# Optimization experiments

Measured on AMD Instinct MI355X. Metric: run time of the kernel, lower is better.

The kernel has to match this reference:

```python
import jax, jax.numpy as jnp
import numpy as np

N = 100000      # n_nodes
E = 1000000     # n_edges (avg degree 10)
D = 64          # input feature dim
LAT = 7         # latent_dim
R = 2           # perturb_rank
H = 2 * LAT     # GCN hidden / dense1 width = 14
P = (LAT + 1) * R  # dense2 width = 16
SP_INV_1 = float(np.log(np.expm1(1.0)))  # softplus_inverse(1.0)


def setup_inputs() -> dict:
    key = jax.random.key(0)
    ks = jax.random.split(key, 10)
    X = jax.random.normal(ks[0], (N, D), dtype=jnp.float32)
    rows = jax.random.randint(ks[1], (E,), 0, N, dtype=jnp.int32)
    cols = jax.random.randint(ks[2], (E,), 0, N, dtype=jnp.int32)
    vals = jax.random.uniform(ks[3], (E,), dtype=jnp.float32)
    s = 0.1
    W1 = jax.random.normal(ks[4], (D, H), dtype=jnp.float32) * s
    W2 = jax.random.normal(ks[5], (H, H), dtype=jnp.float32) * s
    Wd1 = jax.random.normal(ks[6], (H, H), dtype=jnp.float32) * s
    bd1 = jnp.zeros((H,), jnp.float32)
    Wd2 = jax.random.normal(ks[7], (H, P), dtype=jnp.float32) * s
    bd2 = jnp.zeros((P,), jnp.float32)
    return dict(X=X, rows=rows, cols=cols, vals=vals, W1=W1, W2=W2,
                Wd1=Wd1, bd1=bd1, Wd2=Wd2, bd2=bd2)


def reference(X, rows, cols, vals, W1, W2, Wd1, bd1, Wd2, bd2):
    # Sparse adjacency SpMM: (A @ F)[i] = sum_e vals[e] * F[cols[e]] for rows[e]==i
    def spmm(F):
        gathered = vals[:, None] * F[cols]          # [E, d] irregular gather
        return jax.ops.segment_sum(gathered, rows, num_segments=N)

    # GraphConvolution: relu(A @ X @ W)  (keras-gcn order: aggregate then transform)
    h = jax.nn.relu(spmm(X) @ W1)                   # [N, 14]
    h = jax.nn.relu(spmm(h) @ W2)                   # [N, 14]

    param_dist = jnp.tanh(h @ Wd1 + bd1)            # [N, 14]
    param_perturb = jnp.tanh(h @ Wd2 + bd2)         # [N, 16]

    loc = param_dist[:, :LAT]                                      # [N, 7]
    scale_diag = jax.nn.softplus(param_dist[:, LAT:] + SP_INV_1)   # [N, 7]
    perturb_U = param_perturb[:, :LAT * R]                         # [N, 14] (-> [N,7,2])
    perturb_m = param_perturb[:, LAT * R:]                         # [N, 2]

    # MVN-diag-plus-low-rank parameters, concatenated: [N, 7+7+14+2]
    return jnp.concatenate([loc, scale_diag, perturb_U, perturb_m], axis=-1)
```

## Files before the change

### kernel.cpp

```cpp
#include <hip/hip_runtime.h>
#include <hip/hip_fp16.h>
#include <math.h>

constexpr int D     = 64;
constexpr int H     = 14;
constexpr int HP2   = 8;
constexpr int P     = 16;
constexpr int LATc  = 7;
constexpr int OUTW  = 30;
constexpr float SP_INV_1 = 0.5413248546129181f;

__device__ __forceinline__ void pk_atomic_add_f16(__half2* addr, __half2 val) {
    unsigned int bits = *reinterpret_cast<unsigned int*>(&val);
    asm volatile("global_atomic_pk_add_f16 %0, %1, off"
                 :: "v"(addr), "v"(bits) : "memory");
}

__global__ void dense_xw_kernel(const float* __restrict__ X,
                                const float* __restrict__ W1,
                                __half2* __restrict__ XW,
                                __half2* __restrict__ Y1,
                                __half2* __restrict__ Y2, int N) {
    __shared__ float w[D * H];
    for (int i = threadIdx.x; i < D * H; i += blockDim.x) w[i] = W1[i];
    __syncthreads();
    int t = blockIdx.x * blockDim.x + threadIdx.x;
    int n = t >> 1;
    int half = t & 1;
    if (n >= N) return;

    float acc[H];
#pragma unroll
    for (int j = 0; j < H; ++j) acc[j] = 0.f;
    const float4* xr = reinterpret_cast<const float4*>(X + (size_t)n * D) + half * 8;
#pragma unroll
    for (int d4 = 0; d4 < 8; ++d4) {
        float4 x = xr[d4];
        float xs[4] = {x.x, x.y, x.z, x.w};
#pragma unroll
        for (int k = 0; k < 4; ++k) {
            int d = half * 32 + d4 * 4 + k;
#pragma unroll
            for (int j = 0; j < H; ++j) acc[j] = fmaf(xs[k], w[d * H + j], acc[j]);
        }
    }
#pragma unroll
    for (int j = 0; j < H; ++j) acc[j] += __shfl_xor(acc[j], 1);

    __half2 ov[4];
    if (half == 0) {
        ov[0] = __floats2half2_rn(acc[0], acc[1]);
        ov[1] = __floats2half2_rn(acc[2], acc[3]);
        ov[2] = __floats2half2_rn(acc[4], acc[5]);
        ov[3] = __floats2half2_rn(acc[6], acc[7]);
    } else {
        ov[0] = __floats2half2_rn(acc[8], acc[9]);
        ov[1] = __floats2half2_rn(acc[10], acc[11]);
        ov[2] = __floats2half2_rn(acc[12], acc[13]);
        ov[3] = __floats2half2_rn(0.f, 0.f);
    }
    reinterpret_cast<float4*>(XW + (size_t)n * HP2)[half] = *reinterpret_cast<float4*>(ov);

    float4 z = make_float4(0.f, 0.f, 0.f, 0.f);
    reinterpret_cast<float4*>(Y1 + (size_t)n * HP2)[half] = z;
    reinterpret_cast<float4*>(Y2 + (size_t)n * HP2)[half] = z;
}

__global__ void spmm_pk_kernel(const __half2* __restrict__ F,
                               const int* __restrict__ rows,
                               const int* __restrict__ cols,
                               const float* __restrict__ vals,
                               __half2* __restrict__ Y, int E) {
    int idx = blockIdx.x * blockDim.x + threadIdx.x;
    int e = idx >> 3;
    int f = idx & 7;
    if (e >= E || f >= 7) return;
    int r = rows[e];
    int c = cols[e];
    float v = vals[e];
    float2 xf = __half22float2(F[c * HP2 + f]);
    __half2 p = __floats2half2_rn(v * xf.x, v * xf.y);
    pk_atomic_add_f16(&Y[r * HP2 + f], p);
}

__global__ void dense_hw_kernel(const __half2* __restrict__ Y1,
                                const float* __restrict__ W2,
                                __half2* __restrict__ HW, int N) {
    __shared__ float w[H * H];
    for (int i = threadIdx.x; i < H * H; i += blockDim.x) w[i] = W2[i];
    __syncthreads();
    int n = blockIdx.x * blockDim.x + threadIdx.x;
    if (n >= N) return;
    const float4* yr4 = reinterpret_cast<const float4*>(Y1 + (size_t)n * HP2);
    float4 ya = yr4[0], yb = yr4[1];
    __half2 yh[HP2];
    *reinterpret_cast<float4*>(&yh[0]) = ya;
    *reinterpret_cast<float4*>(&yh[4]) = yb;
    float h[H];
#pragma unroll
    for (int k = 0; k < 7; ++k) {
        float2 t = __half22float2(yh[k]);
        h[2 * k]     = fmaxf(t.x, 0.f);
        h[2 * k + 1] = fmaxf(t.y, 0.f);
    }
    float o[H];
#pragma unroll
    for (int j = 0; j < H; ++j) {
        float a = 0.f;
#pragma unroll
        for (int i = 0; i < H; ++i) a = fmaf(h[i], w[i * H + j], a);
        o[j] = a;
    }
    __half2 ov[HP2];
#pragma unroll
    for (int j = 0; j < 7; ++j) ov[j] = __floats2half2_rn(o[2 * j], o[2 * j + 1]);
    ov[7] = __floats2half2_rn(0.f, 0.f);
    float4* dst = reinterpret_cast<float4*>(HW + (size_t)n * HP2);
    dst[0] = *reinterpret_cast<float4*>(&ov[0]);
    dst[1] = *reinterpret_cast<float4*>(&ov[4]);
}

__global__ __launch_bounds__(256) void final_kernel(
        const __half2* __restrict__ Y2,
        const float* __restrict__ Wd1,
        const float* __restrict__ bd1,
        const float* __restrict__ Wd2,
        const float* __restrict__ bd2,
        float* __restrict__ out, int N) {
    __shared__ float wd1[H * H], wd2[H * P], b1[H], b2[P];
    __shared__ float so[256 * OUTW];
    for (int i = threadIdx.x; i < H * H; i += 256) wd1[i] = Wd1[i];
    for (int i = threadIdx.x; i < H * P; i += 256) wd2[i] = Wd2[i];
    if (threadIdx.x < H) b1[threadIdx.x] = bd1[threadIdx.x];
    if (threadIdx.x < P) b2[threadIdx.x] = bd2[threadIdx.x];
    __syncthreads();

    int base = blockIdx.x * 256;
    int n = base + threadIdx.x;
    if (n < N) {
        const float4* yr4 = reinterpret_cast<const float4*>(Y2 + (size_t)n * HP2);
        float4 ya = yr4[0], yb = yr4[1];
        __half2 yh[HP2];
        *reinterpret_cast<float4*>(&yh[0]) = ya;
        *reinterpret_cast<float4*>(&yh[4]) = yb;
        float h[H];
#pragma unroll
        for (int k = 0; k < 7; ++k) {
            float2 t = __half22float2(yh[k]);
            h[2 * k]     = fmaxf(t.x, 0.f);
            h[2 * k + 1] = fmaxf(t.y, 0.f);
        }
        float* so_row = &so[threadIdx.x * OUTW];
        float pd7[LATc];
#pragma unroll
        for (int j = 0; j < H; ++j) {
            float a = b1[j];
#pragma unroll
            for (int i = 0; i < H; ++i) a = fmaf(h[i], wd1[i * H + j], a);
            float t = tanhf(a);
            if (j < LATc) so_row[j] = t;
            else pd7[j - LATc] = t;
        }
#pragma unroll
        for (int k = 0; k < LATc; ++k) {
            float x = pd7[k] + SP_INV_1;
            so_row[LATc + k] = log1pf(expf(x));
        }
#pragma unroll
        for (int j = 0; j < P; ++j) {
            float a = b2[j];
#pragma unroll
            for (int i = 0; i < H; ++i) a = fmaf(h[i], wd2[i * P + j], a);
            so_row[14 + j] = tanhf(a);
        }
    }
    __syncthreads();

    int rowsHere = N - base;
    if (rowsHere > 256) rowsHere = 256;
    if (rowsHere < 0) rowsHere = 0;
    int cnt = rowsHere * OUTW;
    float* obase = out + (size_t)base * OUTW;
    for (int i = threadIdx.x; i < cnt; i += 256) obase[i] = so[i];
}

extern "C" void kernel_launch(void* const* d_in, const int* in_sizes, int n_in,
                              void* d_out, int out_size, void* d_ws, size_t ws_size,
                              hipStream_t stream) {
    const float* X    = (const float*)d_in[0];
    const int*   rows = (const int*)d_in[1];
    const int*   cols = (const int*)d_in[2];
    const float* vals = (const float*)d_in[3];
    const float* W1   = (const float*)d_in[4];
    const float* W2   = (const float*)d_in[5];
    const float* Wd1  = (const float*)d_in[6];
    const float* bd1  = (const float*)d_in[7];
    const float* Wd2  = (const float*)d_in[8];
    const float* bd2  = (const float*)d_in[9];
    float* out = (float*)d_out;

    const int N = in_sizes[0] / D;
    const int E = in_sizes[1];

    __half2* XW = (__half2*)d_ws;
    __half2* HW = XW + (size_t)N * HP2;
    __half2* Y1 = HW + (size_t)N * HP2;
    __half2* Y2 = Y1 + (size_t)N * HP2;

    int blkN  = (N + 255) / 256;
    int blkN2 = (2 * N + 255) / 256;
    long long spmmThreads = (long long)E * 8;
    unsigned blkS = (unsigned)((spmmThreads + 255) / 256);

    dense_xw_kernel<<<blkN2, 256, 0, stream>>>(X, W1, XW, Y1, Y2, N);
    spmm_pk_kernel<<<blkS, 256, 0, stream>>>(XW, rows, cols, vals, Y1, E);
    dense_hw_kernel<<<blkN, 256, 0, stream>>>(Y1, W2, HW, N);
    spmm_pk_kernel<<<blkS, 256, 0, stream>>>(HW, rows, cols, vals, Y2, E);
    final_kernel<<<blkN, 256, 0, stream>>>(Y2, Wd1, bd1, Wd2, bd2, out, N);
}
```

Baseline: 219.0 us.

## Fuse both SpMM passes and dense W2 into persistent kernel with grid barrier

Replaces the two SpMM launches and the dense H×W2 kernel with one persistent kernel sized to occupancy. The kernel runs the first SpMM, waits on a global atomic barrier, then does the second SpMM with the W2 transform computed per edge on the gathered Y1 row instead of a separate pass. This removes two launches and the HW intermediate buffer. In exchange each edge recomputes a 14-wide dot product, reading all 7 half2 of the neighbor row per feature slot. The grid-wide spin barrier assumes every block is co-resident.

```diff
diff --git a/kernel.cpp b/kernel.cpp
--- a/kernel.cpp
+++ b/kernel.cpp
@@ -9,18 +9,24 @@
 constexpr int LATc  = 7;
 constexpr int OUTW  = 30;
 constexpr float SP_INV_1 = 0.5413248546129181f;
+constexpr int BLK   = 256;
 
 __device__ __forceinline__ void pk_atomic_add_f16(__half2* addr, __half2 val) {
     unsigned int bits = *reinterpret_cast<unsigned int*>(&val);
     asm volatile("global_atomic_pk_add_f16 %0, %1, off"
                  :: "v"(addr), "v"(bits) : "memory");
 }
+__device__ __forceinline__ unsigned int ld_agent(const unsigned int* p) {
+    return __hip_atomic_load(p, __ATOMIC_RELAXED, __HIP_MEMORY_SCOPE_AGENT);
+}
 
 __global__ void dense_xw_kernel(const float* __restrict__ X,
                                 const float* __restrict__ W1,
                                 __half2* __restrict__ XW,
                                 __half2* __restrict__ Y1,
-                                __half2* __restrict__ Y2, int N) {
+                                __half2* __restrict__ Y2,
+                                int* __restrict__ bar, int N) {
+    if (blockIdx.x == 0 && threadIdx.x == 0) *bar = 0;
     __shared__ float w[D * H];
     for (int i = threadIdx.x; i < D * H; i += blockDim.x) w[i] = W1[i];
     __syncthreads();
@@ -60,64 +66,82 @@
         ov[3] = __floats2half2_rn(0.f, 0.f);
     }
     reinterpret_cast<float4*>(XW + (size_t)n * HP2)[half] = *reinterpret_cast<float4*>(ov);
-
     float4 z = make_float4(0.f, 0.f, 0.f, 0.f);
     reinterpret_cast<float4*>(Y1 + (size_t)n * HP2)[half] = z;
     reinterpret_cast<float4*>(Y2 + (size_t)n * HP2)[half] = z;
 }
 
-__global__ void spmm_pk_kernel(const __half2* __restrict__ F,
-                               const int* __restrict__ rows,
-                               const int* __restrict__ cols,
-                               const float* __restrict__ vals,
-                               __half2* __restrict__ Y, int E) {
-    int idx = blockIdx.x * blockDim.x + threadIdx.x;
-    int e = idx >> 3;
-    int f = idx & 7;
-    if (e >= E || f >= 7) return;
-    int r = rows[e];
-    int c = cols[e];
-    float v = vals[e];
-    float2 xf = __half22float2(F[c * HP2 + f]);
-    __half2 p = __floats2half2_rn(v * xf.x, v * xf.y);
-    pk_atomic_add_f16(&Y[r * HP2 + f], p);
-}
-
-__global__ void dense_hw_kernel(const __half2* __restrict__ Y1,
-                                const float* __restrict__ W2,
-                                __half2* __restrict__ HW, int N) {
-    __shared__ float w[H * H];
-    for (int i = threadIdx.x; i < H * H; i += blockDim.x) w[i] = W2[i];
-    __syncthreads();
-    int n = blockIdx.x * blockDim.x + threadIdx.x;
-    if (n >= N) return;
-    const float4* yr4 = reinterpret_cast<const float4*>(Y1 + (size_t)n * HP2);
-    float4 ya = yr4[0], yb = yr4[1];
-    __half2 yh[HP2];
-    *reinterpret_cast<float4*>(&yh[0]) = ya;
-    *reinterpret_cast<float4*>(&yh[4]) = yb;
-    float h[H];
-#pragma unroll
-    for (int k = 0; k < 7; ++k) {
-        float2 t = __half22float2(yh[k]);
-        h[2 * k]     = fmaxf(t.x, 0.f);
-        h[2 * k + 1] = fmaxf(t.y, 0.f);
-    }
-    float o[H];
-#pragma unroll
-    for (int j = 0; j < H; ++j) {
-        float a = 0.f;
-#pragma unroll
-        for (int i = 0; i < H; ++i) a = fmaf(h[i], w[i * H + j], a);
-        o[j] = a;
-    }
-    __half2 ov[HP2];
-#pragma unroll
-    for (int j = 0; j < 7; ++j) ov[j] = __floats2half2_rn(o[2 * j], o[2 * j + 1]);
-    ov[7] = __floats2half2_rn(0.f, 0.f);
-    float4* dst = reinterpret_cast<float4*>(HW + (size_t)n * HP2);
-    dst[0] = *reinterpret_cast<float4*>(&ov[0]);
-    dst[1] = *reinterpret_cast<float4*>(&ov[4]);
+__global__ __launch_bounds__(BLK, 4) void spmm_mega_kernel(
+        const __half2* __restrict__ XW,
+        const int* __restrict__ rows,
+        const int* __restrict__ cols,
+        const float* __restrict__ vals,
+        const float* __restrict__ W2,
+        __half2* __restrict__ Y1,
+        __half2* __restrict__ Y2,
+        int* __restrict__ bar,
+        int E, int nblk) {
+    __shared__ float w2s[H * H];
+    for (int i = threadIdx.x; i < H * H; i += BLK) w2s[i] = W2[i];
+    __syncthreads();
+
+    const int tid = blockIdx.x * BLK + threadIdx.x;
+    const int nth = gridDim.x * BLK;
+    const long long tot = (long long)E * 8;
+
+    for (long long i = tid; i < tot; i += nth) {
+        int e = (int)(i >> 3), f = (int)(i & 7);
+        if (f < 7) {
+            int r = rows[e], c = cols[e];
+            float v = vals[e];
+            float2 xf = __half22float2(XW[c * HP2 + f]);
+            __half2 p = __floats2half2_rn(v * xf.x, v * xf.y);
+            pk_atomic_add_f16(&Y1[r * HP2 + f], p);
+        }
+    }
+
+    __syncthreads();
+    if (threadIdx.x == 0) {
+        __hip_atomic_fetch_add(bar, 1, __ATOMIC_ACQ_REL, __HIP_MEMORY_SCOPE_AGENT);
+        while (__hip_atomic_load(bar, __ATOMIC_ACQUIRE, __HIP_MEMORY_SCOPE_AGENT) < nblk)
+            __builtin_amdgcn_s_sleep(1);
+    }
+    __syncthreads();
+
+    const int fslot = tid & 7;
+    float w2a[H], w2b[H];
+    if (fslot < 7) {
+#pragma unroll
+        for (int i = 0; i < H; ++i) {
+            w2a[i] = w2s[i * H + 2 * fslot];
+            w2b[i] = w2s[i * H + 2 * fslot + 1];
+        }
+    }
+    const unsigned int* Y1u = reinterpret_cast<const unsigned int*>(Y1);
+    for (long long i = tid; i < tot; i += nth) {
+        int e = (int)(i >> 3), f = (int)(i & 7);
+        if (f < 7) {
+            int r = rows[e], c = cols[e];
+            float v = vals[e];
+            const unsigned int* yrow = Y1u + (size_t)c * HP2;
+            float h[H];
+#pragma unroll
+            for (int k = 0; k < 7; ++k) {
+                unsigned int u = ld_agent(&yrow[k]);
+                float2 t2 = __half22float2(*reinterpret_cast<__half2*>(&u));
+                h[2 * k]     = fmaxf(t2.x, 0.f);
+                h[2 * k + 1] = fmaxf(t2.y, 0.f);
+            }
+            float a0 = 0.f, a1 = 0.f;
+#pragma unroll
+            for (int i2 = 0; i2 < H; ++i2) {
+                a0 = fmaf(h[i2], w2a[i2], a0);
+                a1 = fmaf(h[i2], w2b[i2], a1);
+            }
+            __half2 p = __floats2half2_rn(v * a0, v * a1);
+            pk_atomic_add_f16(&Y2[r * HP2 + f], p);
+        }
+    }
 }
 
 __global__ __launch_bounds__(256) void final_kernel(
@@ -203,18 +227,23 @@
     const int E = in_sizes[1];
 
     __half2* XW = (__half2*)d_ws;
-    __half2* HW = XW + (size_t)N * HP2;
-    __half2* Y1 = HW + (size_t)N * HP2;
+    __half2* Y1 = XW + (size_t)N * HP2;
     __half2* Y2 = Y1 + (size_t)N * HP2;
+    int* bar = (int*)(Y2 + (size_t)N * HP2);
+
+    int blocksPerCU = 0;
+    (void)hipOccupancyMaxActiveBlocksPerMultiprocessor(
+        &blocksPerCU, (const void*)spmm_mega_kernel, BLK, 0);
+    int numCU = 0;
+    (void)hipDeviceGetAttribute(&numCU, hipDeviceAttributeMultiprocessorCount, 0);
+    int grid = (blocksPerCU > 0 && numCU > 0) ? blocksPerCU * numCU : 1024;
+    if (grid > 4096) grid = 4096;
 
     int blkN  = (N + 255) / 256;
     int blkN2 = (2 * N + 255) / 256;
-    long long spmmThreads = (long long)E * 8;
-    unsigned blkS = (unsigned)((spmmThreads + 255) / 256);
-
-    dense_xw_kernel<<<blkN2, 256, 0, stream>>>(X, W1, XW, Y1, Y2, N);
-    spmm_pk_kernel<<<blkS, 256, 0, stream>>>(XW, rows, cols, vals, Y1, E);
-    dense_hw_kernel<<<blkN, 256, 0, stream>>>(Y1, W2, HW, N);
-    spmm_pk_kernel<<<blkS, 256, 0, stream>>>(HW, rows, cols, vals, Y2, E);
+
+    dense_xw_kernel<<<blkN2, 256, 0, stream>>>(X, W1, XW, Y1, Y2, bar, N);
+    spmm_mega_kernel<<<grid, BLK, 0, stream>>>(XW, rows, cols, vals, W2,
+                                               Y1, Y2, bar, E, grid);
     final_kernel<<<blkN, 256, 0, stream>>>(Y2, Wd1, bd1, Wd2, bd2, out, N);
 }
```

Result: slower. 349.2 us (+59.4%).

## Reorder second GCN layer to aggregate ReLU features before applying W2

Applied to the files above, without the earlier changes.

The second layer now computes A @ relu(Y1) first and multiplies by W2 afterwards, using associativity of (A@h)@W2. The ReLU moves into the SpMM gather, and the W2 transform moves into the final kernel. This removes the separate dense_hw kernel launch and its HW intermediate round trip through memory. Both orderings aggregate 14-wide features, so the SpMM cost stays about the same. The fp16 rounding now lands on different intermediates, which may shift numerical error.

```diff
diff --git a/kernel.cpp b/kernel.cpp
--- a/kernel.cpp
+++ b/kernel.cpp
@@ -60,7 +60,6 @@
         ov[3] = __floats2half2_rn(0.f, 0.f);
     }
     reinterpret_cast<float4*>(XW + (size_t)n * HP2)[half] = *reinterpret_cast<float4*>(ov);
-
     float4 z = make_float4(0.f, 0.f, 0.f, 0.f);
     reinterpret_cast<float4*>(Y1 + (size_t)n * HP2)[half] = z;
     reinterpret_cast<float4*>(Y2 + (size_t)n * HP2)[half] = z;
@@ -83,53 +82,34 @@
     pk_atomic_add_f16(&Y[r * HP2 + f], p);
 }
 
-__global__ void dense_hw_kernel(const __half2* __restrict__ Y1,
-                                const float* __restrict__ W2,
-                                __half2* __restrict__ HW, int N) {
-    __shared__ float w[H * H];
-    for (int i = threadIdx.x; i < H * H; i += blockDim.x) w[i] = W2[i];
-    __syncthreads();
-    int n = blockIdx.x * blockDim.x + threadIdx.x;
-    if (n >= N) return;
-    const float4* yr4 = reinterpret_cast<const float4*>(Y1 + (size_t)n * HP2);
-    float4 ya = yr4[0], yb = yr4[1];
-    __half2 yh[HP2];
-    *reinterpret_cast<float4*>(&yh[0]) = ya;
-    *reinterpret_cast<float4*>(&yh[4]) = yb;
-    float h[H];
-#pragma unroll
-    for (int k = 0; k < 7; ++k) {
-        float2 t = __half22float2(yh[k]);
-        h[2 * k]     = fmaxf(t.x, 0.f);
-        h[2 * k + 1] = fmaxf(t.y, 0.f);
-    }
-    float o[H];
-#pragma unroll
-    for (int j = 0; j < H; ++j) {
-        float a = 0.f;
-#pragma unroll
-        for (int i = 0; i < H; ++i) a = fmaf(h[i], w[i * H + j], a);
-        o[j] = a;
-    }
-    __half2 ov[HP2];
-#pragma unroll
-    for (int j = 0; j < 7; ++j) ov[j] = __floats2half2_rn(o[2 * j], o[2 * j + 1]);
-    ov[7] = __floats2half2_rn(0.f, 0.f);
-    float4* dst = reinterpret_cast<float4*>(HW + (size_t)n * HP2);
-    dst[0] = *reinterpret_cast<float4*>(&ov[0]);
-    dst[1] = *reinterpret_cast<float4*>(&ov[4]);
+__global__ void spmm_relu_kernel(const __half2* __restrict__ Y1,
+                                 const int* __restrict__ rows,
+                                 const int* __restrict__ cols,
+                                 const float* __restrict__ vals,
+                                 __half2* __restrict__ Y2, int E) {
+    int idx = blockIdx.x * blockDim.x + threadIdx.x;
+    int e = idx >> 3;
+    int f = idx & 7;
+    if (e >= E || f >= 7) return;
+    int r = rows[e];
+    int c = cols[e];
+    float v = vals[e];
+    float2 xf = __half22float2(Y1[c * HP2 + f]);
+    __half2 p = __floats2half2_rn(v * fmaxf(xf.x, 0.f), v * fmaxf(xf.y, 0.f));
+    pk_atomic_add_f16(&Y2[r * HP2 + f], p);
 }
 
 __global__ __launch_bounds__(256) void final_kernel(
-        const __half2* __restrict__ Y2,
+        const __half2* __restrict__ Z,
+        const float* __restrict__ W2,
         const float* __restrict__ Wd1,
         const float* __restrict__ bd1,
         const float* __restrict__ Wd2,
         const float* __restrict__ bd2,
         float* __restrict__ out, int N) {
-    __shared__ float wd1[H * H], wd2[H * P], b1[H], b2[P];
+    __shared__ float w2[H * H], wd1[H * H], wd2[H * P], b1[H], b2[P];
     __shared__ float so[256 * OUTW];
-    for (int i = threadIdx.x; i < H * H; i += 256) wd1[i] = Wd1[i];
+    for (int i = threadIdx.x; i < H * H; i += 256) { w2[i] = W2[i]; wd1[i] = Wd1[i]; }
     for (int i = threadIdx.x; i < H * P; i += 256) wd2[i] = Wd2[i];
     if (threadIdx.x < H) b1[threadIdx.x] = bd1[threadIdx.x];
     if (threadIdx.x < P) b2[threadIdx.x] = bd2[threadIdx.x];
@@ -138,17 +118,25 @@
     int base = blockIdx.x * 256;
     int n = base + threadIdx.x;
     if (n < N) {
-        const float4* yr4 = reinterpret_cast<const float4*>(Y2 + (size_t)n * HP2);
-        float4 ya = yr4[0], yb = yr4[1];
-        __half2 yh[HP2];
-        *reinterpret_cast<float4*>(&yh[0]) = ya;
-        *reinterpret_cast<float4*>(&yh[4]) = yb;
+        const float4* zr4 = reinterpret_cast<const float4*>(Z + (size_t)n * HP2);
+        float4 za = zr4[0], zb = zr4[1];
+        __half2 zh[HP2];
+        *reinterpret_cast<float4*>(&zh[0]) = za;
+        *reinterpret_cast<float4*>(&zh[4]) = zb;
+        float z[H];
+#pragma unroll
+        for (int k = 0; k < 7; ++k) {
+            float2 t = __half22float2(zh[k]);
+            z[2 * k]     = t.x;
+            z[2 * k + 1] = t.y;
+        }
         float h[H];
 #pragma unroll
-        for (int k = 0; k < 7; ++k) {
-            float2 t = __half22float2(yh[k]);
-            h[2 * k]     = fmaxf(t.x, 0.f);
-            h[2 * k + 1] = fmaxf(t.y, 0.f);
+        for (int j = 0; j < H; ++j) {
+            float a = 0.f;
+#pragma unroll
+            for (int i = 0; i < H; ++i) a = fmaf(z[i], w2[i * H + j], a);
+            h[j] = fmaxf(a, 0.f);
         }
         float* so_row = &so[threadIdx.x * OUTW];
         float pd7[LATc];
@@ -203,8 +191,7 @@
     const int E = in_sizes[1];
 
     __half2* XW = (__half2*)d_ws;
-    __half2* HW = XW + (size_t)N * HP2;
-    __half2* Y1 = HW + (size_t)N * HP2;
+    __half2* Y1 = XW + (size_t)N * HP2;
     __half2* Y2 = Y1 + (size_t)N * HP2;
 
     int blkN  = (N + 255) / 256;
@@ -214,7 +201,6 @@
 
     dense_xw_kernel<<<blkN2, 256, 0, stream>>>(X, W1, XW, Y1, Y2, N);
     spmm_pk_kernel<<<blkS, 256, 0, stream>>>(XW, rows, cols, vals, Y1, E);
-    dense_hw_kernel<<<blkN, 256, 0, stream>>>(Y1, W2, HW, N);
-    spmm_pk_kernel<<<blkS, 256, 0, stream>>>(HW, rows, cols, vals, Y2, E);
-    final_kernel<<<blkN, 256, 0, stream>>>(Y2, Wd1, bd1, Wd2, bd2, out, N);
-}
+    spmm_relu_kernel<<<blkS, 256, 0, stream>>>(Y1, rows, cols, vals, Y2, E);
+    final_kernel<<<blkN, 256, 0, stream>>>(Y2, W2, Wd1, bd1, Wd2, bd2, out, N);
+}
```

After: 218.4 us. About the same (-0.3%).
